# Kernel optimization log

Measured on AMD Instinct MI355X. Metric: run time of the kernel, lower is better.

Reference implementation:

```python
import jax, jax.numpy as jnp
import numpy as np

N = 100000      # nodes
E = 800000      # edges (nnz of sparse adj)
D_IN = 128      # input feature dim
H = 64          # hidden_units
EMB = 32        # embsize
N_IDX = 50000   # gathered output rows
EPS = 1e-05     # BatchNormalization epsilon


def spmm(rows, cols, vals, x):
    # out[i] = sum_{e: rows[e]==i} vals[e] * x[cols[e]]  == sparse A @ x
    return jax.ops.segment_sum(vals[:, None] * x[cols], rows, num_segments=N)


def batchnorm(x, gamma, beta):
    # training-mode BN over node (batch) axis, matching Keras BatchNormalization
    m = jnp.mean(x, axis=0)
    v = jnp.var(x, axis=0)
    return (x - m) * jax.lax.rsqrt(v + EPS) * gamma + beta


def setup_inputs() -> dict:
    key = jax.random.key(0)
    ks = jax.random.split(key, 16)
    def w(k, fan_in, shape):
        return jax.random.normal(k, shape, dtype=jnp.float32) / np.sqrt(fan_in)
    inp = {
        "features": jax.random.normal(ks[0], (N, D_IN), dtype=jnp.float32),
        "rows": jax.random.randint(ks[1], (E,), 0, N),
        "cols": jax.random.randint(ks[2], (E,), 0, N),
        "vals": jax.random.uniform(ks[3], (E,), dtype=jnp.float32),
        "idx": jax.random.randint(ks[4], (N_IDX,), 0, N),
        # layer 0 (Dense with bias since l==0)
        "Wn0": w(ks[5], D_IN, (D_IN, H)), "bn0": jnp.zeros((H,), jnp.float32),
        "Wg0": w(ks[6], D_IN, (D_IN, H)), "bg0": jnp.zeros((H,), jnp.float32),
        "ab0": jnp.zeros((H,), jnp.float32),  # BiasLayer after SpMM
        "g0": jnp.ones((H,), jnp.float32), "b0": jnp.zeros((H,), jnp.float32),
        # layer 1 (no Dense bias)
        "Wn1": w(ks[7], H, (H, H)),
        "Wg1": w(ks[8], H, (H, H)),
        "ab1": jnp.zeros((H,), jnp.float32),
        "g1": jnp.ones((H,), jnp.float32), "b1": jnp.zeros((H,), jnp.float32),
        # conv_last block (Dense use_bias=False)
        "WnL": w(ks[9], H, (H, EMB)),
        "WgL": w(ks[10], H, (H, EMB)),
        "abL": jnp.zeros((EMB,), jnp.float32),
    }
    return inp


def reference(features, rows, cols, vals, idx,
              Wn0, bn0, Wg0, bg0, ab0, g0, b0,
              Wn1, Wg1, ab1, g1, b1,
              WnL, WgL, abL):
    x = features
    # SAGE layer 0
    x_node = x @ Wn0 + bn0
    x_neigh = x @ Wg0 + bg0
    agg = spmm(rows, cols, vals, x_neigh) + ab0
    x = jax.nn.relu(batchnorm(x_node + agg, g0, b0))
    # SAGE layer 1
    x_node = x @ Wn1
    x_neigh = x @ Wg1
    agg = spmm(rows, cols, vals, x_neigh) + ab1
    x = jax.nn.relu(batchnorm(x_node + agg, g1, b1))
    # conv_last projection to embsize
    x_node = x @ WnL
    x_neigh = x @ WgL
    agg = spmm(rows, cols, vals, x_neigh) + abL
    x = x_node + agg
    return x[idx]
```

## Files before the change

kernel.cpp:

```cpp
#include <hip/hip_runtime.h>

#define NNODES 100000
#define NEDGES 800000
#define DIN    128
#define HID    64
#define EMB    32
#define NIDX   50000
#define BN_EPS 1e-5f

typedef __attribute__((ext_vector_type(8))) short short8;
typedef __attribute__((ext_vector_type(4))) float f32x4;

__device__ inline unsigned short f2bf(float f) {
    unsigned u = __float_as_uint(f);
    unsigned r = u + 0x7FFFu + ((u >> 16) & 1u);
    return (unsigned short)(r >> 16);
}
__device__ inline float bf2f_lo(unsigned u) { return __uint_as_float(u << 16); }
__device__ inline float bf2f_hi(unsigned u) { return __uint_as_float(u & 0xffff0000u); }


__device__ inline void pack_seg(const float* __restrict__ Wn, const float* __restrict__ Wg,
                                unsigned short* __restrict__ Wp, int HOUT, int l2nt, int f) {
    int j = f & 7, lane = (f >> 3) & 63, g = f >> 9;
    int tt = g & ((1 << l2nt) - 1), kb = g >> l2nt;
    int k = kb * 32 + ((lane >> 4) * 8) + j;
    int nn = tt * 16 + (lane & 15);
    float v = (nn < HOUT) ? Wn[k * HOUT + nn] : Wg[k * HOUT + (nn - HOUT)];
    Wp[f] = f2bf(v);
}

__global__ void packall_k(const float* Wn0, const float* Wg0, const float* Wn1,
                          const float* Wg1, const float* WnL, const float* WgL,
                          unsigned short* Wp0, unsigned short* Wp1, unsigned short* WpL) {
    int f = blockIdx.x * 256 + threadIdx.x;
    if (f < 16384)      pack_seg(Wn0, Wg0, Wp0, 64, 3, f);
    else if (f < 24576) pack_seg(Wn1, Wg1, Wp1, 64, 3, f - 16384);
    else if (f < 28672) pack_seg(WnL, WgL, WpL, 32, 2, f - 24576);
}


template <int K, int HOUT, bool AFF, bool XBF, bool HNBF>
__device__ void gemm_body(const void* __restrict__ Xv, const unsigned short* __restrict__ Wp,
                          const float* __restrict__ bnA, const float* __restrict__ bnB,
                          const float* __restrict__ bgA,
                          const float* __restrict__ sums, const float* __restrict__ gamma,
                          const float* __restrict__ beta,
                          float* __restrict__ Hnf, unsigned short* __restrict__ Hnb,
                          unsigned short* __restrict__ Hgb, int n, int blk)
{
    constexpr int NT = 2 * HOUT / 16, NKB = K / 32;
    constexpr int RS = K + 8;
    __shared__ unsigned short Xs[64 * RS];
    __shared__ float sSc[64], sSh[64];

    const int row0 = blk * 64;
    const int t = threadIdx.x;

    if (AFF) {
        if (t < 64) {
            float sum = 0.f, sq = 0.f;
#pragma unroll
            for (int s = 0; s < 8; s++) { sum += sums[s * 128 + t]; sq += sums[s * 128 + 64 + t]; }
            float m = sum / (float)NNODES;
            float var = sq / (float)NNODES - m * m;
            float sc = gamma[t] * rsqrtf(var + BN_EPS);
            sSc[t] = sc; sSh[t] = beta[t] - m * sc;
        }
        __syncthreads();
    }

    for (int li = t; li < 64 * K / 8; li += 256) {
        int r  = li / (K / 8);
        int k8 = (li % (K / 8)) * 8;
        int rr = row0 + r;
        float v[8];
        if (XBF) {
            uint4 u = (rr < n) ? *(const uint4*)((const unsigned short*)Xv + (size_t)rr * K + k8)
                               : make_uint4(0, 0, 0, 0);
            v[0] = bf2f_lo(u.x); v[1] = bf2f_hi(u.x);
            v[2] = bf2f_lo(u.y); v[3] = bf2f_hi(u.y);
            v[4] = bf2f_lo(u.z); v[5] = bf2f_hi(u.z);
            v[6] = bf2f_lo(u.w); v[7] = bf2f_hi(u.w);
        } else {
            const float* Xf = (const float*)Xv;
            float4 a = make_float4(0.f, 0.f, 0.f, 0.f), b = a;
            if (rr < n) {
                a = *(const float4*)&Xf[(size_t)rr * K + k8];
                b = *(const float4*)&Xf[(size_t)rr * K + k8 + 4];
            }
            v[0] = a.x; v[1] = a.y; v[2] = a.z; v[3] = a.w;
            v[4] = b.x; v[5] = b.y; v[6] = b.z; v[7] = b.w;
        }
        if (AFF) {
#pragma unroll
            for (int i = 0; i < 8; i++) v[i] = fmaxf(v[i] * sSc[k8 + i] + sSh[k8 + i], 0.f);
        }
        uint4 o;
        o.x = (unsigned)f2bf(v[0]) | ((unsigned)f2bf(v[1]) << 16);
        o.y = (unsigned)f2bf(v[2]) | ((unsigned)f2bf(v[3]) << 16);
        o.z = (unsigned)f2bf(v[4]) | ((unsigned)f2bf(v[5]) << 16);
        o.w = (unsigned)f2bf(v[6]) | ((unsigned)f2bf(v[7]) << 16);
        *(uint4*)&Xs[r * RS + k8] = o;
    }
    __syncthreads();

    const int wave = t >> 6, lane = t & 63;
    const int q = lane >> 4, mrow = lane & 15;

    f32x4 acc[NT];
#pragma unroll
    for (int i = 0; i < NT; i++) acc[i] = (f32x4){0.f, 0.f, 0.f, 0.f};

    const short8* wp8 = (const short8*)Wp;
#pragma unroll
    for (int kb = 0; kb < NKB; kb++) {
        short8 a = *(const short8*)&Xs[(wave * 16 + mrow) * RS + kb * 32 + q * 8];
#pragma unroll
        for (int tt = 0; tt < NT; tt++) {
            short8 b = wp8[(kb * NT + tt) * 64 + lane];
            acc[tt] = __builtin_amdgcn_mfma_f32_16x16x32_bf16(a, b, acc[tt], 0, 0, 0);
        }
    }

#pragma unroll
    for (int tt = 0; tt < NT; tt++) {
        int nglob = tt * 16 + mrow;
        bool nside = (nglob < HOUT);
        int c = nside ? nglob : (nglob - HOUT);
        float bias = 0.f;
        if (nside) {
            if (bnA) bias += bnA[c];
            if (bnB) bias += bnB[c];
        } else if (bgA) {
            bias += bgA[c];
        }
#pragma unroll
        for (int r = 0; r < 4; r++) {
            int rr = row0 + wave * 16 + q * 4 + r;
            if (rr < n) {
                float o = acc[tt][r] + bias;
                if (nside) {
                    if (HNBF) Hnb[(size_t)rr * HOUT + c] = f2bf(o);
                    else      Hnf[(size_t)rr * HOUT + c] = o;
                } else {
                    Hgb[(size_t)rr * HOUT + c] = f2bf(o);
                }
            }
        }
    }
}

__global__ __launch_bounds__(256) void fused0_k(
    const int* __restrict__ rows, int* __restrict__ cntS, int* __restrict__ rank,
    const float* __restrict__ X, const unsigned short* __restrict__ Wp0,
    const float* __restrict__ bn0, const float* __restrict__ ab0, const float* __restrict__ bg0,
    unsigned short* __restrict__ Hn0b, unsigned short* __restrict__ Hgb, int n, int EB)
{
    if ((int)blockIdx.x < EB) {
        int c = blockIdx.x;
        int e = c * 256 + threadIdx.x;
        if (e < NEDGES) rank[e] = atomicAdd(&cntS[(c & 7) * NNODES + rows[e]], 1);
    } else {
        gemm_body<DIN, HID, false, false, true>(X, Wp0, bn0, ab0, bg0,
            nullptr, nullptr, nullptr, nullptr, Hn0b, Hgb, n, blockIdx.x - EB);
    }
}

template <int K, int HOUT, bool AFF, bool XBF, bool HNBF>
__global__ __launch_bounds__(256) void gemm_k(
    const void* __restrict__ X, const unsigned short* __restrict__ Wp,
    const float* __restrict__ bnA, const float* __restrict__ bnB, const float* __restrict__ bgA,
    const float* __restrict__ sums, const float* __restrict__ gamma, const float* __restrict__ beta,
    float* __restrict__ Hnf, unsigned short* __restrict__ Hnb, unsigned short* __restrict__ Hgb, int n)
{
    gemm_body<K, HOUT, AFF, XBF, HNBF>(X, Wp, bnA, bnB, bgA, sums, gamma, beta,
                                       Hnf, Hnb, Hgb, n, blockIdx.x);
}


__global__ void sumscan_k(const int* __restrict__ cntS, int* __restrict__ base,
                          int* __restrict__ cnt, int* __restrict__ part, int n) {
    __shared__ int sm[256];
    int t = threadIdx.x, r = blockIdx.x * 256 + t;
    int c = 0;
    if (r < n) {
        int b[8];
#pragma unroll
        for (int s = 0; s < 8; s++) { b[s] = c; c += cntS[s * NNODES + r]; }
        cnt[r] = c;
        *(int4*)&base[r * 8]     = make_int4(b[0], b[1], b[2], b[3]);
        *(int4*)&base[r * 8 + 4] = make_int4(b[4], b[5], b[6], b[7]);
    }
    sm[t] = c;
    __syncthreads();
    for (int off = 128; off > 0; off >>= 1) {
        if (t < off) sm[t] += sm[t + off];
        __syncthreads();
    }
    if (t == 0) part[blockIdx.x] = sm[0];
}

__global__ void scan2_k(int* part, int nb) {
    __shared__ int s[512];
    int t = threadIdx.x;
    int v = (t < nb) ? part[t] : 0;
    s[t] = v;
    __syncthreads();
    for (int off = 1; off < 512; off <<= 1) {
        int a = (t >= off) ? s[t - off] : 0;
        __syncthreads();
        s[t] += a;
        __syncthreads();
    }
    if (t < nb) part[t] = s[t] - v;
}

__global__ void scan3_k(const int* __restrict__ cnt, const int* __restrict__ part,
                        int* __restrict__ rowptr, int n, int E) {
    __shared__ int s[256];
    int t = threadIdx.x;
    int i = blockIdx.x * 256 + t;
    int v = (i < n) ? cnt[i] : 0;
    s[t] = v;
    __syncthreads();
    for (int off = 1; off < 256; off <<= 1) {
        int a = (t >= off) ? s[t - off] : 0;
        __syncthreads();
        s[t] += a;
        __syncthreads();
    }
    if (i < n) rowptr[i] = part[blockIdx.x] + s[t] - v;
    if (i == 0) rowptr[n] = E;
}

__global__ void scattermark_k(const int* __restrict__ rows, const int* __restrict__ cols,
                              const float* __restrict__ vals, const int* __restrict__ rank,
                              const int* __restrict__ base, const int* __restrict__ rowptr,
                              int2* __restrict__ cs, const int* __restrict__ idx,
                              int* __restrict__ mark, int EB) {
    if ((int)blockIdx.x < EB) {
        int e = blockIdx.x * 256 + threadIdx.x;
        if (e < NEDGES) {
            int r = rows[e];
            int s = (e >> 8) & 7;
            cs[rowptr[r] + base[r * 8 + s] + rank[e]] = make_int2(cols[e], __float_as_int(vals[e]));
        }
    } else {
        int j = ((int)blockIdx.x - EB) * 256 + threadIdx.x;
        if (j < NIDX) mark[idx[j]] = 1;
    }
}


template <int HH, bool STATS, bool SBF, bool MARKED>
__global__ __launch_bounds__(256) void spmm_k(
    const int* __restrict__ rowptr, const int2* __restrict__ cs,
    const unsigned short* __restrict__ Hgb, void* __restrict__ Sv,
    float* __restrict__ stats, const int* __restrict__ mark, int n)
{
    constexpr int L  = HH / 4;
    constexpr int GP = 256 / L;
    const int lane = threadIdx.x % L;
    const int g = threadIdx.x / L;
    const int gid = blockIdx.x * GP + g;
    const int ngroups = gridDim.x * GP;
    const int c0 = lane * 4;

    float4 sum = make_float4(0.f, 0.f, 0.f, 0.f);
    float4 sq  = make_float4(0.f, 0.f, 0.f, 0.f);
    for (int row = gid; row < n; row += ngroups) {
        if (MARKED && !mark[row]) continue;
        int e0 = rowptr[row], e1 = rowptr[row + 1];
        float4 a0, a1 = make_float4(0.f, 0.f, 0.f, 0.f);
        if (SBF) {
            uint2 h = *(const uint2*)((const unsigned short*)Sv + (size_t)row * HH + c0);
            a0 = make_float4(bf2f_lo(h.x), bf2f_hi(h.x), bf2f_lo(h.y), bf2f_hi(h.y));
        } else {
            a0 = *(const float4*)((const float*)Sv + (size_t)row * HH + c0);
        }
        int e = e0;
        for (; e + 1 < e1; e += 2) {
            int2 p0 = cs[e], p1 = cs[e + 1];
            float v0 = __int_as_float(p0.y), v1 = __int_as_float(p1.y);
            uint2 h0 = *(const uint2*)&Hgb[(size_t)p0.x * HH + c0];
            uint2 h1 = *(const uint2*)&Hgb[(size_t)p1.x * HH + c0];
            a0.x += v0 * bf2f_lo(h0.x); a0.y += v0 * bf2f_hi(h0.x);
            a0.z += v0 * bf2f_lo(h0.y); a0.w += v0 * bf2f_hi(h0.y);
            a1.x += v1 * bf2f_lo(h1.x); a1.y += v1 * bf2f_hi(h1.x);
            a1.z += v1 * bf2f_lo(h1.y); a1.w += v1 * bf2f_hi(h1.y);
        }
        if (e < e1) {
            int2 p = cs[e];
            float v = __int_as_float(p.y);
            uint2 h = *(const uint2*)&Hgb[(size_t)p.x * HH + c0];
            a0.x += v * bf2f_lo(h.x); a0.y += v * bf2f_hi(h.x);
            a0.z += v * bf2f_lo(h.y); a0.w += v * bf2f_hi(h.y);
        }
        float4 acc = make_float4(a0.x + a1.x, a0.y + a1.y, a0.z + a1.z, a0.w + a1.w);
        if (SBF) {
            uint2 o;
            o.x = (unsigned)f2bf(acc.x) | ((unsigned)f2bf(acc.y) << 16);
            o.y = (unsigned)f2bf(acc.z) | ((unsigned)f2bf(acc.w) << 16);
            *(uint2*)((unsigned short*)Sv + (size_t)row * HH + c0) = o;
        } else {
            *(float4*)((float*)Sv + (size_t)row * HH + c0) = acc;
        }
        if (STATS) {
            sum.x += acc.x; sum.y += acc.y; sum.z += acc.z; sum.w += acc.w;
            sq.x += acc.x * acc.x; sq.y += acc.y * acc.y;
            sq.z += acc.z * acc.z; sq.w += acc.w * acc.w;
        }
    }

    if constexpr (STATS) {
        __shared__ float rs[GP][HH];
        __shared__ float rq[GP][HH];
        *(float4*)&rs[g][c0] = sum;
        *(float4*)&rq[g][c0] = sq;
        __syncthreads();
        if (threadIdx.x < HH) {
            float a = 0.f, b = 0.f;
            for (int w = 0; w < GP; w++) { a += rs[w][threadIdx.x]; b += rq[w][threadIdx.x]; }
            int stripe = blockIdx.x & 7;
            atomicAdd(&stats[stripe * 128 + threadIdx.x], a);
            atomicAdd(&stats[stripe * 128 + HH + threadIdx.x], b);
        }
    }
}

__global__ void gather_k(const float* __restrict__ S, const int* __restrict__ idx,
                         float* __restrict__ out, int total4) {
    int j = blockIdx.x * 256 + threadIdx.x;
    if (j < total4) {
        int r = j / (EMB / 4), c4 = (j % (EMB / 4)) * 4;
        *(float4*)&out[(size_t)j * 4] = *(const float4*)&S[(size_t)idx[r] * EMB + c4];
    }
}


extern "C" void kernel_launch(void* const* d_in, const int* in_sizes, int n_in,
                              void* d_out, int out_size, void* d_ws, size_t ws_size,
                              hipStream_t stream) {
    const float* features = (const float*)d_in[0];
    const int*   rows     = (const int*)d_in[1];
    const int*   cols     = (const int*)d_in[2];
    const float* vals     = (const float*)d_in[3];
    const int*   idx      = (const int*)d_in[4];
    const float* Wn0 = (const float*)d_in[5];
    const float* bn0 = (const float*)d_in[6];
    const float* Wg0 = (const float*)d_in[7];
    const float* bg0 = (const float*)d_in[8];
    const float* ab0 = (const float*)d_in[9];
    const float* g0  = (const float*)d_in[10];
    const float* b0  = (const float*)d_in[11];
    const float* Wn1 = (const float*)d_in[12];
    const float* Wg1 = (const float*)d_in[13];
    const float* ab1 = (const float*)d_in[14];
    const float* g1  = (const float*)d_in[15];
    const float* b1  = (const float*)d_in[16];
    const float* WnL = (const float*)d_in[17];
    const float* WgL = (const float*)d_in[18];
    const float* abL = (const float*)d_in[19];
    float* out = (float*)d_out;

    float*          HnLf = (float*)d_ws;
    unsigned short* nA   = (unsigned short*)(HnLf + (size_t)NNODES * EMB);
    unsigned short* nB   = nA + (size_t)NNODES * HID;
    unsigned short* Hgb  = nB + (size_t)NNODES * HID;
    int*   part   = (int*)(Hgb + (size_t)NNODES * HID);
    int*   rowptr = part + 1024;
    int*   cnt    = rowptr + (NNODES + 4);
    int*   rank   = cnt + NNODES;
    int*   base   = rank + NEDGES;
    int2*  cs     = (int2*)(base + 8 * NNODES);
    unsigned short* Wp0 = (unsigned short*)(cs + NEDGES);
    unsigned short* Wp1 = Wp0 + 16384;
    unsigned short* WpL = Wp1 + 8192;
    int*   cntS  = (int*)(WpL + 4096);
    float* stats = (float*)(cntS + 8 * NNODES);
    int*   mark  = (int*)(stats + 2304);
    float* sums0 = stats;
    float* sums1 = stats + 1024;
    size_t zbytes = (size_t)8 * NNODES * 4 + 2304 * 4 + (size_t)NNODES * 4;

    hipMemsetAsync(cntS, 0, zbytes, stream);

    const int EB  = (NEDGES + 255) / 256;
    const int NB  = (NNODES + 255) / 256;
    const int GBm = (NNODES + 63) / 64;
    const int MB  = (NIDX + 255) / 256;

    packall_k<<<112, 256, 0, stream>>>(Wn0, Wg0, Wn1, Wg1, WnL, WgL, Wp0, Wp1, WpL);

    fused0_k<<<EB + GBm, 256, 0, stream>>>(rows, cntS, rank, features, Wp0,
                                           bn0, ab0, bg0, nA, Hgb, NNODES, EB);

    sumscan_k<<<NB, 256, 0, stream>>>(cntS, base, cnt, part, NNODES);
    scan2_k<<<1, 512, 0, stream>>>(part, NB);
    scan3_k<<<NB, 256, 0, stream>>>(cnt, part, rowptr, NNODES, NEDGES);
    scattermark_k<<<EB + MB, 256, 0, stream>>>(rows, cols, vals, rank, base, rowptr,
                                               cs, idx, mark, EB);

    spmm_k<HID, true, true, false><<<1600, 256, 0, stream>>>(rowptr, cs, Hgb, nA, sums0, nullptr, NNODES);

    gemm_k<HID, HID, true, true, true><<<GBm, 256, 0, stream>>>(
        nA, Wp1, ab1, nullptr, nullptr, sums0, g0, b0, nullptr, nB, Hgb, NNODES);
    spmm_k<HID, true, true, false><<<1600, 256, 0, stream>>>(rowptr, cs, Hgb, nB, sums1, nullptr, NNODES);

    gemm_k<HID, EMB, true, true, false><<<GBm, 256, 0, stream>>>(
        nB, WpL, abL, nullptr, nullptr, sums1, g1, b1, HnLf, nullptr, Hgb, NNODES);
    spmm_k<EMB, false, false, true><<<1600, 256, 0, stream>>>(rowptr, cs, Hgb, HnLf, nullptr, mark, NNODES);

    gather_k<<<(NIDX * EMB / 4 + 255) / 256, 256, 0, stream>>>(HnLf, idx, out, NIDX * EMB / 4);
}
```

Measured before the change: 314.4 us.

## Replace global-atomic CSR build with two-level bucketed partition sort

Replaces the COO-to-CSR conversion, which used per-edge global atomics on striped counters plus a three-kernel scan, with a two-pass bucket partition. Edges are first histogrammed per chunk into 64-row buckets in shared memory, prefix-summed, and scattered into a bucket-ordered buffer. A per-bucket kernel then sorts each bucket by row with shared-memory atomics. This removes global atomic contention and the large counter memset. The cost is an extra int4 edge buffer and a serial per-bucket prefix kernel. Edge order within a row becomes nondeterministic.

```diff
diff --git a/kernel.cpp b/kernel.cpp
--- a/kernel.cpp
+++ b/kernel.cpp
@@ -7,6 +7,10 @@
 #define EMB    32
 #define NIDX   50000
 #define BN_EPS 1e-5f
+
+#define NCHK 256
+#define EC   (NEDGES / NCHK)
+#define NB   ((NNODES + 63) / 64)
 
 typedef __attribute__((ext_vector_type(8))) short short8;
 typedef __attribute__((ext_vector_type(4))) float f32x4;
@@ -37,6 +41,97 @@
     if (f < 16384)      pack_seg(Wn0, Wg0, Wp0, 64, 3, f);
     else if (f < 24576) pack_seg(Wn1, Wg1, Wp1, 64, 3, f - 16384);
     else if (f < 28672) pack_seg(WnL, WgL, WpL, 32, 2, f - 24576);
+}
+
+
+__global__ __launch_bounds__(256) void bhist_k(const int* __restrict__ rows,
+                                               int* __restrict__ Bcnt,
+                                               const int* __restrict__ idx,
+                                               int* __restrict__ mark) {
+    if ((int)blockIdx.x >= NCHK) {
+        int j = ((int)blockIdx.x - NCHK) * 256 + threadIdx.x;
+        if (j < NIDX) mark[idx[j]] = 1;
+        return;
+    }
+    __shared__ int hist[NB];
+    int t = threadIdx.x, blk = blockIdx.x;
+    for (int b = t; b < NB; b += 256) hist[b] = 0;
+    __syncthreads();
+    for (int i = t; i < EC; i += 256)
+        atomicAdd(&hist[rows[blk * EC + i] >> 6], 1);
+    __syncthreads();
+    for (int b = t; b < NB; b += 256) Bcnt[b * NCHK + blk] = hist[b];
+}
+
+__global__ void bprefix_k(const int* __restrict__ Bcnt, int* __restrict__ BcntT,
+                          int* __restrict__ bTot) {
+    int b = blockIdx.x * 256 + threadIdx.x;
+    if (b >= NB) return;
+    int run = 0;
+    for (int j = 0; j < NCHK; j++) {
+        BcntT[j * NB + b] = run;
+        run += Bcnt[b * NCHK + j];
+    }
+    bTot[b] = run;
+}
+
+__global__ void bscan_k(const int* __restrict__ bTot, int* __restrict__ bBase) {
+    __shared__ int s[256];
+    int t = threadIdx.x;
+    int v[7], loc = 0;
+#pragma unroll
+    for (int i = 0; i < 7; i++) {
+        int ix = t * 7 + i;
+        v[i] = loc;
+        loc += (ix < NB) ? bTot[ix] : 0;
+    }
+    s[t] = loc;
+    __syncthreads();
+    for (int off = 1; off < 256; off <<= 1) {
+        int a = (t >= off) ? s[t - off] : 0;
+        __syncthreads();
+        s[t] += a;
+        __syncthreads();
+    }
+    int base = s[t] - loc;
+#pragma unroll
+    for (int i = 0; i < 7; i++) {
+        int ix = t * 7 + i;
+        if (ix < NB) bBase[ix] = base + v[i];
+    }
+    if (t == 255) bBase[NB] = NEDGES;
+}
+
+__global__ __launch_bounds__(256) void bfinal_k(const int4* __restrict__ ebuf,
+                                                const int* __restrict__ bBase,
+                                                int* __restrict__ rowptr,
+                                                int2* __restrict__ cs) {
+    __shared__ int hist[64], sc[64], cur[64];
+    int b = blockIdx.x, t = threadIdx.x;
+    int e0 = bBase[b], e1 = bBase[b + 1];
+    int r0 = b << 6;
+    if (t < 64) hist[t] = 0;
+    __syncthreads();
+    for (int i = e0 + t; i < e1; i += 256)
+        atomicAdd(&hist[ebuf[i].x & 63], 1);
+    __syncthreads();
+    if (t == 0) {
+        int run = e0;
+        for (int j = 0; j < 64; j++) { sc[j] = run; run += hist[j]; }
+    }
+    __syncthreads();
+    if (t < 64) {
+        cur[t] = sc[t];
+        int r = r0 + t;
+        if (r < NNODES) rowptr[r] = sc[t];
+    }
+    if (b == NB - 1 && t == 0) rowptr[NNODES] = NEDGES;
+    __syncthreads();
+    for (int i = e0 + t; i < e1; i += 256) {
+        int4 v = ebuf[i];
+        int p = atomicAdd(&cur[v.x & 63], 1);
+        cs[p] = make_int2(v.y, v.z);
+    }
 }
 
 
@@ -151,19 +246,28 @@
     }
 }
 
-__global__ __launch_bounds__(256) void fused0_k(
-    const int* __restrict__ rows, int* __restrict__ cntS, int* __restrict__ rank,
+__global__ __launch_bounds__(256) void part_gemm0_k(
+    const int* __restrict__ rows, const int* __restrict__ cols,
+    const float* __restrict__ vals, const int* __restrict__ BcntT,
+    const int* __restrict__ bBase, int4* __restrict__ ebuf,
     const float* __restrict__ X, const unsigned short* __restrict__ Wp0,
     const float* __restrict__ bn0, const float* __restrict__ ab0, const float* __restrict__ bg0,
-    unsigned short* __restrict__ Hn0b, unsigned short* __restrict__ Hgb, int n, int EB)
+    unsigned short* __restrict__ Hn0b, unsigned short* __restrict__ Hgb, int n)
 {
-    if ((int)blockIdx.x < EB) {
-        int c = blockIdx.x;
-        int e = c * 256 + threadIdx.x;
-        if (e < NEDGES) rank[e] = atomicAdd(&cntS[(c & 7) * NNODES + rows[e]], 1);
+    if ((int)blockIdx.x < NCHK) {
+        __shared__ int cur[NB];
+        int t = threadIdx.x, blk = blockIdx.x;
+        for (int b = t; b < NB; b += 256) cur[b] = bBase[b] + BcntT[blk * NB + b];
+        __syncthreads();
+        for (int i = t; i < EC; i += 256) {
+            int e = blk * EC + i;
+            int r = rows[e];
+            int p = atomicAdd(&cur[r >> 6], 1);
+            ebuf[p] = make_int4(r, cols[e], __float_as_int(vals[e]), 0);
+        }
     } else {
         gemm_body<DIN, HID, false, false, true>(X, Wp0, bn0, ab0, bg0,
-            nullptr, nullptr, nullptr, nullptr, Hn0b, Hgb, n, blockIdx.x - EB);
+            nullptr, nullptr, nullptr, nullptr, Hn0b, Hgb, n, blockIdx.x - NCHK);
     }
 }
 
@@ -176,80 +280,6 @@
 {
     gemm_body<K, HOUT, AFF, XBF, HNBF>(X, Wp, bnA, bnB, bgA, sums, gamma, beta,
                                        Hnf, Hnb, Hgb, n, blockIdx.x);
-}
-
-
-__global__ void sumscan_k(const int* __restrict__ cntS, int* __restrict__ base,
-                          int* __restrict__ cnt, int* __restrict__ part, int n) {
-    __shared__ int sm[256];
-    int t = threadIdx.x, r = blockIdx.x * 256 + t;
-    int c = 0;
-    if (r < n) {
-        int b[8];
-#pragma unroll
-        for (int s = 0; s < 8; s++) { b[s] = c; c += cntS[s * NNODES + r]; }
-        cnt[r] = c;
-        *(int4*)&base[r * 8]     = make_int4(b[0], b[1], b[2], b[3]);
-        *(int4*)&base[r * 8 + 4] = make_int4(b[4], b[5], b[6], b[7]);
-    }
-    sm[t] = c;
-    __syncthreads();
-    for (int off = 128; off > 0; off >>= 1) {
-        if (t < off) sm[t] += sm[t + off];
-        __syncthreads();
-    }
-    if (t == 0) part[blockIdx.x] = sm[0];
-}
-
-__global__ void scan2_k(int* part, int nb) {
-    __shared__ int s[512];
-    int t = threadIdx.x;
-    int v = (t < nb) ? part[t] : 0;
-    s[t] = v;
-    __syncthreads();
-    for (int off = 1; off < 512; off <<= 1) {
-        int a = (t >= off) ? s[t - off] : 0;
-        __syncthreads();
-        s[t] += a;
-        __syncthreads();
-    }
-    if (t < nb) part[t] = s[t] - v;
-}
-
-__global__ void scan3_k(const int* __restrict__ cnt, const int* __restrict__ part,
-                        int* __restrict__ rowptr, int n, int E) {
-    __shared__ int s[256];
-    int t = threadIdx.x;
-    int i = blockIdx.x * 256 + t;
-    int v = (i < n) ? cnt[i] : 0;
-    s[t] = v;
-    __syncthreads();
-    for (int off = 1; off < 256; off <<= 1) {
-        int a = (t >= off) ? s[t - off] : 0;
-        __syncthreads();
-        s[t] += a;
-        __syncthreads();
-    }
-    if (i < n) rowptr[i] = part[blockIdx.x] + s[t] - v;
-    if (i == 0) rowptr[n] = E;
-}
-
-__global__ void scattermark_k(const int* __restrict__ rows, const int* __restrict__ cols,
-                              const float* __restrict__ vals, const int* __restrict__ rank,
-                              const int* __restrict__ base, const int* __restrict__ rowptr,
-                              int2* __restrict__ cs, const int* __restrict__ idx,
-                              int* __restrict__ mark, int EB) {
-    if ((int)blockIdx.x < EB) {
-        int e = blockIdx.x * 256 + threadIdx.x;
-        if (e < NEDGES) {
-            int r = rows[e];
-            int s = (e >> 8) & 7;
-            cs[rowptr[r] + base[r * 8 + s] + rank[e]] = make_int2(cols[e], __float_as_int(vals[e]));
-        }
-    } else {
-        int j = ((int)blockIdx.x - EB) * 256 + threadIdx.x;
-        if (j < NIDX) mark[idx[j]] = 1;
-    }
 }
 
 
@@ -368,39 +398,36 @@
     unsigned short* nA   = (unsigned short*)(HnLf + (size_t)NNODES * EMB);
     unsigned short* nB   = nA + (size_t)NNODES * HID;
     unsigned short* Hgb  = nB + (size_t)NNODES * HID;
-    int*   part   = (int*)(Hgb + (size_t)NNODES * HID);
-    int*   rowptr = part + 1024;
-    int*   cnt    = rowptr + (NNODES + 4);
-    int*   rank   = cnt + NNODES;
-    int*   base   = rank + NEDGES;
-    int2*  cs     = (int2*)(base + 8 * NNODES);
-    unsigned short* Wp0 = (unsigned short*)(cs + NEDGES);
+    int4*  ebuf  = (int4*)(Hgb + (size_t)NNODES * HID);
+    int2*  cs    = (int2*)(ebuf + NEDGES);
+    int*   rowptr = (int*)(cs + NEDGES);
+    int*   Bcnt  = rowptr + (NNODES + 4);
+    int*   BcntT = Bcnt + NB * NCHK;
+    int*   bTot  = BcntT + NCHK * NB;
+    int*   bBase = bTot + 1568;
+    unsigned short* Wp0 = (unsigned short*)(bBase + 1568);
     unsigned short* Wp1 = Wp0 + 16384;
     unsigned short* WpL = Wp1 + 8192;
-    int*   cntS  = (int*)(WpL + 4096);
-    float* stats = (float*)(cntS + 8 * NNODES);
+    float* stats = (float*)(WpL + 4096);
     int*   mark  = (int*)(stats + 2304);
     float* sums0 = stats;
     float* sums1 = stats + 1024;
-    size_t zbytes = (size_t)8 * NNODES * 4 + 2304 * 4 + (size_t)NNODES * 4;
-
-    hipMemsetAsync(cntS, 0, zbytes, stream);
-
-    const int EB  = (NEDGES + 255) / 256;
-    const int NB  = (NNODES + 255) / 256;
+    size_t zbytes = 2304 * 4 + (size_t)NNODES * 4;
+
+    hipMemsetAsync(stats, 0, zbytes, stream);
+
     const int GBm = (NNODES + 63) / 64;
     const int MB  = (NIDX + 255) / 256;
 
     packall_k<<<112, 256, 0, stream>>>(Wn0, Wg0, Wn1, Wg1, WnL, WgL, Wp0, Wp1, WpL);
 
-    fused0_k<<<EB + GBm, 256, 0, stream>>>(rows, cntS, rank, features, Wp0,
-                                           bn0, ab0, bg0, nA, Hgb, NNODES, EB);
-
-    sumscan_k<<<NB, 256, 0, stream>>>(cntS, base, cnt, part, NNODES);
-    scan2_k<<<1, 512, 0, stream>>>(part, NB);
-    scan3_k<<<NB, 256, 0, stream>>>(cnt, part, rowptr, NNODES, NEDGES);
-    scattermark_k<<<EB + MB, 256, 0, stream>>>(rows, cols, vals, rank, base, rowptr,
-                                               cs, idx, mark, EB);
+    bhist_k<<<NCHK + MB, 256, 0, stream>>>(rows, Bcnt, idx, mark);
+    bprefix_k<<<7, 256, 0, stream>>>(Bcnt, BcntT, bTot);
+    bscan_k<<<1, 256, 0, stream>>>(bTot, bBase);
+    part_gemm0_k<<<NCHK + GBm, 256, 0, stream>>>(rows, cols, vals, BcntT, bBase, ebuf,
+                                                 features, Wp0, bn0, ab0, bg0,
+                                                 nA, Hgb, NNODES);
+    bfinal_k<<<NB, 256, 0, stream>>>(ebuf, bBase, rowptr, cs);
 
     spmm_k<HID, true, true, false><<<1600, 256, 0, stream>>>(rowptr, cs, Hgb, nA, sums0, nullptr, NNODES);
 
```

After: 287.2 us. -8.6%, faster.
